# Kernel optimization log

Measured on AMD Instinct MI355X. Metric: run time of the kernel, lower is better.

## Reference

```python
import jax, jax.numpy as jnp
import numpy as np

NUM_HEADS = 8
EPS = 1e-5

def layer_norm(x, g, b):
    m = jnp.mean(x, axis=-1, keepdims=True)
    v = jnp.mean(jnp.square(x - m), axis=-1, keepdims=True)
    return (x - m) * jax.lax.rsqrt(v + EPS) * g + b

def setup_inputs() -> dict:
    key = jax.random.key(0)
    ks = jax.random.split(key, 16)
    B, C_enc, C_dec = 2, 512, 256
    H = W = D = 16
    d_ff = 4 * C_dec
    s = 0.02
    inp = {
        'encoder_feat': jax.random.normal(ks[0], (B, C_enc, H, W, D), jnp.float32),
        'decoder_feat': jax.random.normal(ks[1], (B, C_dec, H, W, D), jnp.float32),
        # projections stored as (in, out)
        'Wq': jax.random.normal(ks[2], (C_dec, C_dec), jnp.float32) * s,
        'bq': jnp.zeros((C_dec,), jnp.float32),
        'Wk': jax.random.normal(ks[3], (C_enc, C_dec), jnp.float32) * s,
        'bk': jnp.zeros((C_dec,), jnp.float32),
        'Wv': jax.random.normal(ks[4], (C_enc, C_dec), jnp.float32) * s,
        'bv': jnp.zeros((C_dec,), jnp.float32),
        'Wo': jax.random.normal(ks[5], (C_dec, C_dec), jnp.float32) * s,
        'bo': jnp.zeros((C_dec,), jnp.float32),
        'g_enc': jnp.ones((C_enc,), jnp.float32),
        'b_enc': jnp.zeros((C_enc,), jnp.float32),
        'g_dec': jnp.ones((C_dec,), jnp.float32),
        'b_dec': jnp.zeros((C_dec,), jnp.float32),
        'g_out': jnp.ones((C_dec,), jnp.float32),
        'b_out': jnp.zeros((C_dec,), jnp.float32),
        'W1': jax.random.normal(ks[6], (C_dec, d_ff), jnp.float32) * s,
        'b1': jnp.zeros((d_ff,), jnp.float32),
        'W2': jax.random.normal(ks[7], (d_ff, C_dec), jnp.float32) * s,
        'b2': jnp.zeros((C_dec,), jnp.float32),
    }
    return inp

def reference(encoder_feat, decoder_feat, Wq, bq, Wk, bk, Wv, bv, Wo, bo,
              g_enc, b_enc, g_dec, b_dec, g_out, b_out, W1, b1, W2, b2):
    B, C_dec, H, W, D = decoder_feat.shape
    h = NUM_HEADS
    hd = C_dec // h
    scale = hd ** -0.5
    # flatten spatial dims -> sequences [B, S, C]
    enc_seq = encoder_feat.reshape(B, encoder_feat.shape[1], -1).transpose(0, 2, 1)
    dec_seq = decoder_feat.reshape(B, C_dec, -1).transpose(0, 2, 1)
    enc_n = layer_norm(enc_seq, g_enc, b_enc)
    dec_n = layer_norm(dec_seq, g_dec, b_dec)
    Sq = dec_n.shape[1]
    Sk = enc_n.shape[1]
    Q = (dec_n @ Wq + bq).reshape(B, Sq, h, hd).transpose(0, 2, 1, 3)
    K = (enc_n @ Wk + bk).reshape(B, Sk, h, hd).transpose(0, 2, 1, 3)
    V = (enc_n @ Wv + bv).reshape(B, Sk, h, hd).transpose(0, 2, 1, 3)
    attn = jnp.einsum('bhqd,bhkd->bhqk', Q, K) * scale
    attn = jax.nn.softmax(attn, axis=-1)
    out = jnp.einsum('bhqk,bhkd->bhqd', attn, V)
    out = out.transpose(0, 2, 1, 3).reshape(B, Sq, C_dec)
    out = out @ Wo + bo
    out = dec_seq + out
    ffn = jax.nn.gelu(layer_norm(out, g_out, b_out) @ W1 + b1, approximate=False) @ W2 + b2
    out = out + ffn
    return out.transpose(0, 2, 1).reshape(B, C_dec, H, W, D)
```

## Files before the change

### kernel.cpp

```cpp
#include <hip/hip_runtime.h>
#include <hip/hip_bf16.h>
#include <math.h>
#include <stdint.h>

typedef __hip_bfloat16 bf16;
typedef __attribute__((ext_vector_type(8))) short short8;
typedef __attribute__((ext_vector_type(4))) short short4v;
typedef __attribute__((ext_vector_type(4))) float f32x4;
typedef __attribute__((ext_vector_type(4))) unsigned int uint32x4;
typedef __attribute__((ext_vector_type(2))) unsigned int uint32x2;

#define B_   2
#define S_   4096
#define CE   512
#define CD   256
#define DFF  1024
#define NH   8
#define HD   32

static __device__ __forceinline__ float b2f(bf16 x) { return __bfloat162float(x); }
static __device__ __forceinline__ bf16  f2b(float x) { return __float2bfloat16(x); }
static __device__ __forceinline__ short f2bs(float x) {
  bf16 h = f2b(x); return __builtin_bit_cast(short, h);
}
static __device__ __forceinline__ float s2f(short x) {
  return b2f(__builtin_bit_cast(bf16, x));
}
static __device__ __forceinline__ bool is_f32(const unsigned* graw) {
  return graw[0] == 0x3F800000u;
}

static __device__ __forceinline__ float exp2_(float x) {
#if __has_builtin(__builtin_amdgcn_exp2f)
  return __builtin_amdgcn_exp2f(x);
#else
  float r; asm("v_exp_f32 %0, %1" : "=v"(r) : "v"(x)); return r;
#endif
}
static __device__ __forceinline__ unsigned cvt_pk_bf16(float lo, float hi) {
  unsigned r;
  asm("v_cvt_pk_bf16_f32 %0, %1, %2" : "=v"(r) : "v"(lo), "v"(hi));
  return r;
}
static __device__ __forceinline__ void perm32(unsigned& a, unsigned& b) {
#if __has_builtin(__builtin_amdgcn_permlane32_swap)
  uint32x2 r = __builtin_amdgcn_permlane32_swap(a, b, false, false);
  a = r[0]; b = r[1];
#else
  asm("v_permlane32_swap_b32 %0, %1" : "+v"(a), "+v"(b));
#endif
}
static __device__ __forceinline__ void perm16(unsigned& a, unsigned& b) {
#if __has_builtin(__builtin_amdgcn_permlane16_swap)
  uint32x2 r = __builtin_amdgcn_permlane16_swap(a, b, false, false);
  a = r[0]; b = r[1];
#else
  asm("v_permlane16_swap_b32 %0, %1" : "+v"(a), "+v"(b));
#endif
}

#define GLD16(gptr, lptr) \
  __builtin_amdgcn_global_load_lds( \
      (const __attribute__((address_space(1))) unsigned int*)(gptr), \
      (__attribute__((address_space(3))) unsigned int*)(lptr), 16, 0, 0)

#define WAITVM(N) asm volatile("s_waitcnt vmcnt(" #N ")" ::: "memory")
#define BAR() __builtin_amdgcn_s_barrier()

struct PrepTab {
  const void* tsrc[6];
  bf16* tdst[6];
  int tK[6], tsStr[6], tdStr[6];
  float tscl[6];
  int tbase[7];
  const void* csrc[14];
  bf16* cdst[14];
  float cscl[14];
  int coff[15];
};

__global__ __launch_bounds__(256) void prep_kernel(
    PrepTab p, const unsigned* __restrict__ graw) {
  __shared__ bf16 tile[32][33];
  bool f32i = is_f32(graw);
  int blk = blockIdx.x;
  if (blk < p.tbase[6]) {
    int j = 0;
    #pragma unroll 1
    while (blk >= p.tbase[j + 1]) ++j;
    int local = blk - p.tbase[j];
    int ktiles = p.tK[j] >> 5;
    int nt = local / ktiles, kt = local - nt * ktiles;
    int k0 = kt * 32, n0 = nt * 32;
    const void* src = p.tsrc[j];
    bf16* dst = p.tdst[j];
    int sStr = p.tsStr[j], dStr = p.tdStr[j];
    float scl = p.tscl[j];
    int t = threadIdx.x;
    int tc = t & 31, tr = t >> 5;
    #pragma unroll
    for (int i = 0; i < 32; i += 8) {
      size_t idx = (size_t)(k0 + tr + i) * sStr + n0 + tc;
      float v = f32i ? ((const float*)src)[idx] : b2f(((const bf16*)src)[idx]);
      tile[tr + i][tc] = f2b(v * scl);
    }
    __syncthreads();
    #pragma unroll
    for (int i = 0; i < 32; i += 8)
      dst[(size_t)(n0 + tr + i) * dStr + k0 + tc] = tile[tc][tr + i];
  } else {
    int idx = (blk - p.tbase[6]) * 256 + threadIdx.x;
    int e4 = idx * 4;
    if (e4 >= p.coff[14]) return;
    int j = 0;
    #pragma unroll 1
    while (e4 >= p.coff[j + 1]) ++j;
    int local = e4 - p.coff[j];
    float v0, v1, v2, v3;
    if (f32i) {
      float4 f = *(const float4*)((const float*)p.csrc[j] + local);
      v0 = f.x; v1 = f.y; v2 = f.z; v3 = f.w;
    } else {
      short4v h = *(const short4v*)((const short*)p.csrc[j] + local);
      v0 = s2f(h[0]); v1 = s2f(h[1]); v2 = s2f(h[2]); v3 = s2f(h[3]);
    }
    float scl = p.cscl[j];
    short4v o;
    o[0] = f2bs(v0 * scl); o[1] = f2bs(v1 * scl);
    o[2] = f2bs(v2 * scl); o[3] = f2bs(v3 * scl);
    *(short4v*)((short*)p.cdst[j] + local) = o;
  }
}

struct LNCfg {
  const bf16 *x, *g, *bt;
  bf16 *xn, *xt;
  int C;
};

template<int CC, bool XT>
static __device__ __forceinline__ void ln_tile_body(
    const LNCfg& T, int b, int s0, short* sT, short* sG, short* sBt) {
  constexpr int P = CC + 8;
  constexpr int NJ = CC / 64;
  int t = threadIdx.x;
  if (t < CC / 8)      *(short8*)&sG[t * 8] = ((const short8*)T.g)[t];
  else if (t < CC / 4) *(short8*)&sBt[(t - CC/8) * 8] = ((const short8*)T.bt)[t - CC/8];

  int cg = t >> 2;
  int sq = (t & 3) * 8;
  const short* xg = (const short*)T.x + (size_t)b * CC * S_ + s0 + sq;
  short8 ld[NJ];
  #pragma unroll
  for (int ci = 0; ci < NJ; ++ci)
    ld[ci] = *(const short8*)(xg + (size_t)(ci * 64 + cg) * S_);
  #pragma unroll
  for (int ci = 0; ci < NJ; ++ci) {
    int c = ci * 64 + cg;
    #pragma unroll
    for (int j = 0; j < 8; ++j) {
      int s = sq + j;
      sT[s * P + (c ^ ((s & 24) << 1))] = ld[ci][j];
    }
  }
  __syncthreads();

  int w = t >> 6, l = t & 63;
  int grp = l >> 3, k = l & 7;
  int s = w * 8 + grp;
  int Z = (s & 24) << 1;
  short8 vals[NJ];
  float sum = 0.f, sq2 = 0.f;
  #pragma unroll
  for (int j = 0; j < NJ; ++j) {
    vals[j] = *(const short8*)&sT[s * P + j * 64 + ((k * 8) ^ Z)];
    #pragma unroll
    for (int i = 0; i < 8; ++i) {
      float v = s2f(vals[j][i]);
      sum += v; sq2 += v * v;
    }
  }
  #pragma unroll
  for (int off = 1; off < 8; off <<= 1) {
    sum += __shfl_xor(sum, off);
    sq2 += __shfl_xor(sq2, off);
  }
  float mean = sum * (1.f / CC);
  float rstd = rsqrtf(sq2 * (1.f / CC) - mean * mean + 1e-5f);
  size_t ro = ((size_t)b * S_ + s0 + s) * CC;
  #pragma unroll
  for (int j = 0; j < NJ; ++j) {
    int c0 = j * 64 + k * 8;
    short8 gv = *(const short8*)&sG[c0];
    short8 bv = *(const short8*)&sBt[c0];
    short8 o;
    #pragma unroll
    for (int i = 0; i < 8; ++i) {
      float v = s2f(vals[j][i]);
      o[i] = f2bs((v - mean) * rstd * s2f(gv[i]) + s2f(bv[i]));
    }
    *(short8*)((short*)T.xn + ro + c0) = o;
    if (XT) *(short8*)((short*)T.xt + ro + c0) = vals[j];
  }
}

__global__ __launch_bounds__(256) void ln_tile_kernel(LNCfg e, LNCfg d) {
  __shared__ __align__(16) short sT[32 * 520];
  __shared__ __align__(16) short sG[512], sBt[512];
  int gb = blockIdx.x;
  int local = gb & 255;
  int b = local >> 7, s0 = (local & 127) * 32;
  if (gb < 256) ln_tile_body<512, false>(e, b, s0, sT, sG, sBt);
  else          ln_tile_body<256, true>(d, b, s0, sT, sG, sBt);
}

__global__ __launch_bounds__(256) void ln_rows_kernel(
    const float* __restrict__ x, const bf16* __restrict__ g,
    const bf16* __restrict__ bt, bf16* __restrict__ xn, int C) {
  int wave = threadIdx.x >> 6, lane = threadIdx.x & 63;
  int row = blockIdx.x * 4 + wave;
  float4 v = *(const float4*)(x + (size_t)row * 256 + lane * 4);
  float sum = v.x + v.y + v.z + v.w;
  float sq = v.x * v.x + v.y * v.y + v.z * v.z + v.w * v.w;
  #pragma unroll
  for (int off = 1; off < 64; off <<= 1) {
    sum += __shfl_xor(sum, off);
    sq  += __shfl_xor(sq, off);
  }
  float mean = sum * (1.f / 256.f);
  float rstd = rsqrtf(sq * (1.f / 256.f) - mean * mean + 1e-5f);
  short4v gg = *(const short4v*)((const short*)g + lane * 4);
  short4v bb = *(const short4v*)((const short*)bt + lane * 4);
  short4v o;
  o[0] = f2bs((v.x - mean) * rstd * s2f(gg[0]) + s2f(bb[0]));
  o[1] = f2bs((v.y - mean) * rstd * s2f(gg[1]) + s2f(bb[1]));
  o[2] = f2bs((v.z - mean) * rstd * s2f(gg[2]) + s2f(bb[2]));
  o[3] = f2bs((v.w - mean) * rstd * s2f(gg[3]) + s2f(bb[3]));
  *(short4v*)((short*)xn + (size_t)row * 256 + lane * 4) = o;
}

__global__ __launch_bounds__(256) void gemm_mfma_kernel(
    const bf16* __restrict__ A, const bf16* __restrict__ Wt,
    const bf16* __restrict__ bias, int M, int N, int K,
    const bf16* __restrict__ resid_bf, const float* __restrict__ resid_f,
    bf16* __restrict__ out_bf, float* __restrict__ out_f,
    void* __restrict__ out_t, const unsigned* __restrict__ graw,
    int act, int resid_mode, int out_mode) {
  __shared__ __align__(16) short sA[3][128 * 32];
  __shared__ __align__(16) short sB[3][64 * 32];
  int m0 = blockIdx.y * 128, n0 = blockIdx.x * 64;
  int t = threadIdx.x;
  int w = t >> 6;
  int wm = w >> 1, wn = w & 1;
  int n16 = t & 15, quad = (t & 63) >> 4;
  int srow = t >> 2, skg = (t & 3) * 8;

  f32x4 acc[4][2] = {};
  const short* Ag = (const short*)A;
  const short* Wg = (const short*)Wt;
  const short* a0p = Ag + (size_t)(m0 + srow) * K + skg;
  const short* a1p = Ag + (size_t)(m0 + 64 + srow) * K + skg;
  const short* wp  = Wg + (size_t)(n0 + srow) * K + skg;

  auto stage = [&](int buf, int kk) {
    GLD16(a0p + kk, (char*)sA[buf] + t * 16);
    GLD16(a1p + kk, (char*)sA[buf] + t * 16 + 4096);
    GLD16(wp + kk,  (char*)sB[buf] + t * 16);
  };
  int nt = K >> 5;
  stage(0, 0);
  stage(1, 32);
  WAITVM(3);
  BAR();

  for (int ti = 0; ti < nt; ++ti) {
    int cur = ti % 3;
    bool pf = (ti + 2) < nt;
    if (pf) stage((ti + 2) % 3, (ti + 2) * 32);
    short8 af[4], bfr[2];
    #pragma unroll
    for (int ms = 0; ms < 4; ++ms)
      af[ms] = *(const short8*)&sA[cur][(wm * 64 + ms * 16 + n16) * 32 + quad * 8];
    #pragma unroll
    for (int ns = 0; ns < 2; ++ns)
      bfr[ns] = *(const short8*)&sB[cur][(wn * 32 + ns * 16 + n16) * 32 + quad * 8];
    #pragma unroll
    for (int ms = 0; ms < 4; ++ms)
      #pragma unroll
      for (int ns = 0; ns < 2; ++ns)
        acc[ms][ns] = __builtin_amdgcn_mfma_f32_16x16x32_bf16(
            af[ms], bfr[ns], acc[ms][ns], 0, 0, 0);
    if (pf) WAITVM(3); else WAITVM(0);
    BAR();
  }

  #pragma unroll
  for (int ms = 0; ms < 4; ++ms) {
    #pragma unroll
    for (int ns = 0; ns < 2; ++ns) {
      int col = n0 + wn * 32 + ns * 16 + n16;
      float bv = b2f(bias[col]);
      #pragma unroll
      for (int r = 0; r < 4; ++r) {
        int row = m0 + wm * 64 + ms * 16 + quad * 4 + r;
        float c = acc[ms][ns][r] + bv;
        if (act == 1) c = 0.5f * c * (1.f + erff(c * 0.70710678118654752f));
        size_t off = (size_t)row * N + col;
        if (resid_mode == 1)      c += b2f(resid_bf[off]);
        else if (resid_mode == 2) c += resid_f[off];
        if (out_f) out_f[off] = c;
        else       out_bf[off] = f2b(c);
      }
    }
  }
}

__global__ __launch_bounds__(256) void gemm64_mfma_kernel(
    const bf16* __restrict__ A, const bf16* __restrict__ Wt,
    const bf16* __restrict__ bias, int M, int N, int K,
    const bf16* __restrict__ resid_bf, const float* __restrict__ resid_f,
    bf16* __restrict__ out_bf, float* __restrict__ out_f,
    void* __restrict__ out_t, const unsigned* __restrict__ graw,
    int act, int resid_mode, int out_mode) {
  __shared__ __align__(16) short sA[3][64 * 32];
  __shared__ __align__(16) short sB[3][64 * 32];
  int m0 = blockIdx.y * 64, n0 = blockIdx.x * 64;
  int t = threadIdx.x;
  int w = t >> 6;
  int wm = w >> 1, wn = w & 1;
  int n16 = t & 15, quad = (t & 63) >> 4;
  int srow = t >> 2, skg = (t & 3) * 8;

  f32x4 acc[2][2] = {};
  const short* Ag = (const short*)A;
  const short* Wg = (const short*)Wt;
  const short* ap = Ag + (size_t)(m0 + srow) * K + skg;
  const short* wp = Wg + (size_t)(n0 + srow) * K + skg;

  auto stage = [&](int buf, int kk) {
    GLD16(ap + kk, (char*)sA[buf] + t * 16);
    GLD16(wp + kk, (char*)sB[buf] + t * 16);
  };
  int nt = K >> 5;
  stage(0, 0);
  stage(1, 32);
  WAITVM(2);
  BAR();

  for (int ti = 0; ti < nt; ++ti) {
    int cur = ti % 3;
    bool pf = (ti + 2) < nt;
    if (pf) stage((ti + 2) % 3, (ti + 2) * 32);
    short8 af[2], bfr[2];
    #pragma unroll
    for (int ms = 0; ms < 2; ++ms)
      af[ms] = *(const short8*)&sA[cur][(wm * 32 + ms * 16 + n16) * 32 + quad * 8];
    #pragma unroll
    for (int ns = 0; ns < 2; ++ns)
      bfr[ns] = *(const short8*)&sB[cur][(wn * 32 + ns * 16 + n16) * 32 + quad * 8];
    #pragma unroll
    for (int ms = 0; ms < 2; ++ms)
      #pragma unroll
      for (int ns = 0; ns < 2; ++ns)
        acc[ms][ns] = __builtin_amdgcn_mfma_f32_16x16x32_bf16(
            af[ms], bfr[ns], acc[ms][ns], 0, 0, 0);
    if (pf) WAITVM(2); else WAITVM(0);
    BAR();
  }

  if (out_mode == 3) {
    bool isf32 = is_f32(graw);
    #pragma unroll
    for (int ms = 0; ms < 2; ++ms) {
      int row0 = m0 + wm * 32 + ms * 16 + quad * 4;
      int bb = row0 >> 12, s = row0 & (S_ - 1);
      #pragma unroll
      for (int ns = 0; ns < 2; ++ns) {
        int col = n0 + wn * 32 + ns * 16 + n16;
        float bv = b2f(bias[col]);
        float cv[4];
        #pragma unroll
        for (int r = 0; r < 4; ++r)
          cv[r] = acc[ms][ns][r] + bv + resid_f[(size_t)(row0 + r) * N + col];
        size_t oidx = ((size_t)bb * CD + col) * S_ + s;
        if (isf32) {
          float4 v4 = {cv[0], cv[1], cv[2], cv[3]};
          *(float4*)((float*)out_t + oidx) = v4;
        } else {
          short4v v;
          #pragma unroll
          for (int r = 0; r < 4; ++r) v[r] = f2bs(cv[r]);
          *(short4v*)((bf16*)out_t + oidx) = v;
        }
      }
    }
    return;
  }

  #pragma unroll
  for (int ms = 0; ms < 2; ++ms) {
    #pragma unroll
    for (int ns = 0; ns < 2; ++ns) {
      int col = n0 + wn * 32 + ns * 16 + n16;
      float bv = b2f(bias[col]);
      #pragma unroll
      for (int r = 0; r < 4; ++r) {
        int row = m0 + wm * 32 + ms * 16 + quad * 4 + r;
        float c = acc[ms][ns][r] + bv;
        if (act == 1) c = 0.5f * c * (1.f + erff(c * 0.70710678118654752f));
        size_t off = (size_t)row * N + col;
        if (resid_mode == 1)      c += b2f(resid_bf[off]);
        else if (resid_mode == 2) c += resid_f[off];
        if (out_f) out_f[off] = c;
        else       out_bf[off] = f2b(c);
      }
    }
  }
}

__global__ __launch_bounds__(256) void qkv_kernel(
    const bf16* __restrict__ dec_n, const bf16* __restrict__ enc_n,
    const bf16* __restrict__ Wqt, const bf16* __restrict__ Wkvt,
    const bf16* __restrict__ bq, const bf16* __restrict__ bkv,
    bf16* __restrict__ Qm, bf16* __restrict__ Km, bf16* __restrict__ VT) {
  __shared__ __align__(16) short sA[3][64 * 32];
  __shared__ __align__(16) short sB[3][64 * 32];
  bool isQ = blockIdx.x < 4;
  const short* Ag = (const short*)(isQ ? dec_n : enc_n);
  const short* Wg = (const short*)(isQ ? Wqt : Wkvt);
  const bf16* bias = isQ ? bq : bkv;
  int K = isQ ? CD : CE;
  int n0 = isQ ? blockIdx.x * 64 : (blockIdx.x - 4) * 64;
  int m0 = blockIdx.y * 64;
  int t = threadIdx.x;
  int w = t >> 6;
  int wm = w >> 1, wn = w & 1;
  int n16 = t & 15, quad = (t & 63) >> 4;
  int srow = t >> 2, skg = (t & 3) * 8;

  f32x4 acc[2][2] = {};
  const short* ap = Ag + (size_t)(m0 + srow) * K + skg;
  const short* wp = Wg + (size_t)(n0 + srow) * K + skg;
  auto stage = [&](int buf, int kk) {
    GLD16(ap + kk, (char*)sA[buf] + t * 16);
    GLD16(wp + kk, (char*)sB[buf] + t * 16);
  };
  int nt = K >> 5;
  stage(0, 0);
  stage(1, 32);
  WAITVM(2);
  BAR();

  for (int ti = 0; ti < nt; ++ti) {
    int cur = ti % 3;
    bool pf = (ti + 2) < nt;
    if (pf) stage((ti + 2) % 3, (ti + 2) * 32);
    short8 af[2], bfr[2];
    #pragma unroll
    for (int ms = 0; ms < 2; ++ms)
      af[ms] = *(const short8*)&sA[cur][(wm * 32 + ms * 16 + n16) * 32 + quad * 8];
    #pragma unroll
    for (int ns = 0; ns < 2; ++ns)
      bfr[ns] = *(const short8*)&sB[cur][(wn * 32 + ns * 16 + n16) * 32 + quad * 8];
    #pragma unroll
    for (int ms = 0; ms < 2; ++ms)
      #pragma unroll
      for (int ns = 0; ns < 2; ++ns)
        acc[ms][ns] = __builtin_amdgcn_mfma_f32_16x16x32_bf16(
            af[ms], bfr[ns], acc[ms][ns], 0, 0, 0);
    if (pf) WAITVM(2); else WAITVM(0);
    BAR();
  }

  if (!isQ && n0 >= 256) {
    #pragma unroll
    for (int ms = 0; ms < 2; ++ms) {
      int row0 = m0 + wm * 32 + ms * 16 + quad * 4;
      int bb = row0 >> 12, s = row0 & (S_ - 1);
      #pragma unroll
      for (int ns = 0; ns < 2; ++ns) {
        int col = n0 + wn * 32 + ns * 16 + n16;
        float bv = b2f(bias[col]);
        short4v v;
        #pragma unroll
        for (int r = 0; r < 4; ++r) v[r] = f2bs(acc[ms][ns][r] + bv);
        *(short4v*)(VT + ((size_t)bb * CD + col - 256) * S_ + s) = v;
      }
    }
    return;
  }
  bf16* outp = isQ ? Qm : Km;
  #pragma unroll
  for (int ms = 0; ms < 2; ++ms) {
    #pragma unroll
    for (int ns = 0; ns < 2; ++ns) {
      int col = n0 + wn * 32 + ns * 16 + n16;
      float bv = b2f(bias[col]);
      #pragma unroll
      for (int r = 0; r < 4; ++r) {
        int row = m0 + wm * 32 + ms * 16 + quad * 4 + r;
        outp[(size_t)row * CD + col] = f2b(acc[ms][ns][r] + bv);
      }
    }
  }
}

__global__ __launch_bounds__(256) void attn_mfma_kernel(
    const bf16* __restrict__ Qm, const bf16* __restrict__ Km,
    const bf16* __restrict__ VT, float* __restrict__ Op0,
    float* __restrict__ Op1, float* __restrict__ Lp) {
  __shared__ __align__(16) short sKf[2][4][64][8];
  __shared__ __align__(16) short sVt[2][32][64];
  int b = blockIdx.z, h = blockIdx.y >> 1, half = blockIdx.y & 1;
  int q0 = blockIdx.x * 64;
  int t = threadIdx.x;
  int w = t >> 6, l = t & 63;
  int n = l & 15, quad = l >> 4;
  size_t bh = ((size_t)b * S_) * CD + h * HD;
  const short* kg = (const short*)Km + bh + (size_t)(w * 16 + n) * CD + quad * 8;
  const short* vtg = (const short*)VT +
      (size_t)(b * CD + h * HD + w * 8 + (l >> 3)) * S_ + ((l & 7) ^ ((l >> 3) & 7)) * 8;

  short8 qf = *(const short8*)((const short*)Qm + bh +
                               (size_t)(q0 + w * 16 + n) * CD + quad * 8);
  short8 ones8;
  #pragma unroll
  for (int i = 0; i < 8; ++i) ones8[i] = (short)0x3F80;

  f32x4 o0 = {0.f, 0.f, 0.f, 0.f}, o1 = {0.f, 0.f, 0.f, 0.f};
  f32x4 ol = {0.f, 0.f, 0.f, 0.f};

  auto stageKV = [&](int buf, int kk) {
    GLD16(kg + (size_t)kk * CD, &sKf[buf][w][l][0]);
    GLD16(vtg + kk, (short*)sVt[buf] + w * 512 + l * 8);
  };

  int kbeg = half * (S_ / 2), kend = kbeg + S_ / 2;
  stageKV(0, kbeg);
  WAITVM(0);
  BAR();
  int cur = 0;
  for (int k0 = kbeg; k0 < kend; k0 += 64) {
    if (k0 + 64 < kend) stageKV(cur ^ 1, k0 + 64);

    f32x4 sc[4];
    __builtin_amdgcn_s_setprio(1);
    #pragma unroll
    for (int st = 0; st < 4; ++st) {
      short8 kf = *(const short8*)&sKf[cur][st][l][0];
      f32x4 z = {0.f, 0.f, 0.f, 0.f};
      sc[st] = __builtin_amdgcn_mfma_f32_16x16x32_bf16(kf, qf, z, 0, 0, 0);
    }
    __builtin_amdgcn_s_setprio(0);

    unsigned Wd[4][2];
    #pragma unroll
    for (int st = 0; st < 4; ++st) {
      Wd[st][0] = cvt_pk_bf16(exp2_(sc[st][0]), exp2_(sc[st][1]));
      Wd[st][1] = cvt_pk_bf16(exp2_(sc[st][2]), exp2_(sc[st][3]));
    }
    uint32x4 pw0, pw1;
    #pragma unroll
    for (int m = 0; m < 2; ++m) {
      unsigned a0 = Wd[0][m], b0 = Wd[1][m];
      perm32(a0, b0); perm16(a0, b0);
      pw0[m] = a0; pw0[2 + m] = b0;
      unsigned a1 = Wd[2][m], b1 = Wd[3][m];
      perm32(a1, b1); perm16(a1, b1);
      pw1[m] = a1; pw1[2 + m] = b1;
    }
    short8 pf0 = __builtin_bit_cast(short8, pw0);
    short8 pf1 = __builtin_bit_cast(short8, pw1);

    int p80 = quad ^ (n & 7), p81 = (4 + quad) ^ (n & 7);
    short8 v00 = *(const short8*)&sVt[cur][n][p80 * 8];
    short8 v01 = *(const short8*)&sVt[cur][n][p81 * 8];
    short8 v10 = *(const short8*)&sVt[cur][16 + n][p80 * 8];
    short8 v11 = *(const short8*)&sVt[cur][16 + n][p81 * 8];

    __builtin_amdgcn_s_setprio(1);
    o0 = __builtin_amdgcn_mfma_f32_16x16x32_bf16(pf0, v00, o0, 0, 0, 0);
    o1 = __builtin_amdgcn_mfma_f32_16x16x32_bf16(pf0, v10, o1, 0, 0, 0);
    ol = __builtin_amdgcn_mfma_f32_16x16x32_bf16(pf0, ones8, ol, 0, 0, 0);
    o0 = __builtin_amdgcn_mfma_f32_16x16x32_bf16(pf1, v01, o0, 0, 0, 0);
    o1 = __builtin_amdgcn_mfma_f32_16x16x32_bf16(pf1, v11, o1, 0, 0, 0);
    ol = __builtin_amdgcn_mfma_f32_16x16x32_bf16(pf1, ones8, ol, 0, 0, 0);
    __builtin_amdgcn_s_setprio(0);

    WAITVM(0);
    BAR();
    cur ^= 1;
  }

  float* Opb = half ? Op1 : Op0;
  size_t pb = (size_t)b * S_;
  #pragma unroll
  for (int r = 0; r < 4; ++r) {
    int q = q0 + w * 16 + quad * 4 + r;
    float* orow = Opb + (pb + q) * CD + h * HD;
    orow[n]      = o0[r];
    orow[16 + n] = o1[r];
    if (n == 0) Lp[((size_t)(b * 2 + half) * S_ + q) * NH + h] = ol[r];
  }
}

__global__ __launch_bounds__(256) void attn_combine_kernel(
    const float* __restrict__ Op0, const float* __restrict__ Op1,
    const float* __restrict__ Lp, bf16* __restrict__ Am) {
  int idx = blockIdx.x * 256 + threadIdx.x;
  int c = (idx * 4) & (CD - 1);
  int bs = (idx * 4) >> 8;
  int s = bs & (S_ - 1), b = bs >> 12;
  int h = c >> 5;
  size_t row = (size_t)b * S_ + s;
  float l0 = Lp[((size_t)(b * 2 + 0) * S_ + s) * NH + h];
  float l1 = Lp[((size_t)(b * 2 + 1) * S_ + s) * NH + h];
  float inv = 1.f / (l0 + l1);
  float4 a = *(const float4*)&Op0[row * CD + c];
  float4 d = *(const float4*)&Op1[row * CD + c];
  short4v v;
  v[0] = f2bs((a.x + d.x) * inv);
  v[1] = f2bs((a.y + d.y) * inv);
  v[2] = f2bs((a.z + d.z) * inv);
  v[3] = f2bs((a.w + d.w) * inv);
  *(short4v*)&Am[row * CD + c] = v;
}

extern "C" void kernel_launch(void* const* d_in, const int* in_sizes, int n_in,
                              void* d_out, int out_size, void* d_ws, size_t ws_size,
                              hipStream_t stream) {
  const float kscale = 0.25503486f;
  const unsigned* graw = (const unsigned*)d_in[10];
  char* base = (char*)d_ws;
  size_t pos = 256;

  auto alloc = [&](size_t bytes) {
    char* p = base + pos; pos = (pos + bytes + 255) & ~(size_t)255; return p;
  };
  int cidx[14] = {0, 1, 3, 5, 7, 9, 10, 11, 12, 13, 14, 15, 17, 19};
  bf16* conv[20] = {};
  for (int k = 0; k < 14; ++k) {
    int i = cidx[k];
    conv[i] = (bf16*)alloc((size_t)2 * in_sizes[i]);
  }
  bf16* Wqt  = (bf16*)alloc((size_t)CD * CD * 2);
  bf16* Wkvt = (bf16*)alloc((size_t)CE * CE * 2);
  bf16* Wot  = (bf16*)alloc((size_t)CD * CD * 2);
  bf16* W1t  = (bf16*)alloc((size_t)DFF * CD * 2);
  bf16* W2t  = (bf16*)alloc((size_t)CD * DFF * 2);
  bf16* bkv  = (bf16*)alloc((size_t)CE * 2);
  conv[5] = bkv;
  conv[7] = bkv + CD;

  bf16*  enc_n = (bf16*) alloc((size_t)B_ * S_ * CE * 2);
  bf16*  dec_n = (bf16*) alloc((size_t)B_ * S_ * CD * 2);
  bf16*  Qm    = (bf16*) alloc((size_t)B_ * S_ * CD * 2);
  bf16*  Km    = (bf16*) alloc((size_t)B_ * S_ * CD * 2);
  bf16*  VT    = (bf16*) alloc((size_t)B_ * S_ * CD * 2);
  float* outm  = (float*)alloc((size_t)B_ * S_ * CD * 4);
  bf16*  hid   = (bf16*) alloc((size_t)B_ * S_ * DFF * 2);
  float* Lp    = (float*)alloc((size_t)B_ * 2 * S_ * NH * 4);
  bf16*  Am    = dec_n;
  bf16*  ln2   = Km;
  bf16*  dec_t = (bf16*)hid;
  float* Op0   = outm;
  float* Op1   = (float*)enc_n;

  PrepTab p;
  p.tsrc[0] = d_in[2];  p.tdst[0] = Wqt;            p.tK[0] = CD;  p.tsStr[0] = CD;  p.tdStr[0] = CD;  p.tscl[0] = kscale;
  p.tsrc[1] = d_in[4];  p.tdst[1] = Wkvt;           p.tK[1] = CE;  p.tsStr[1] = CD;  p.tdStr[1] = CE;  p.tscl[1] = 1.0f;
  p.tsrc[2] = d_in[6];  p.tdst[2] = Wkvt + CD * CE; p.tK[2] = CE;  p.tsStr[2] = CD;  p.tdStr[2] = CE;  p.tscl[2] = 1.0f;
  p.tsrc[3] = d_in[8];  p.tdst[3] = Wot;            p.tK[3] = CD;  p.tsStr[3] = CD;  p.tdStr[3] = CD;  p.tscl[3] = 1.0f;
  p.tsrc[4] = d_in[16]; p.tdst[4] = W1t;            p.tK[4] = CD;  p.tsStr[4] = DFF; p.tdStr[4] = CD;  p.tscl[4] = 1.0f;
  p.tsrc[5] = d_in[18]; p.tdst[5] = W2t;            p.tK[5] = DFF; p.tsStr[5] = CD;  p.tdStr[5] = DFF; p.tscl[5] = 1.0f;
  int tN[6] = {CD, CD, CD, CD, DFF, CD};
  p.tbase[0] = 0;
  for (int j = 0; j < 6; ++j)
    p.tbase[j + 1] = p.tbase[j] + (tN[j] / 32) * (p.tK[j] / 32);
  int coff = 0;
  for (int k = 0; k < 14; ++k) {
    int i = cidx[k];
    p.csrc[k] = d_in[i];
    p.cdst[k] = conv[i];
    p.cscl[k] = (i == 3) ? kscale : 1.0f;
    p.coff[k] = coff;
    coff += in_sizes[i];
  }
  p.coff[14] = coff;
  int prep_blocks = p.tbase[6] + (coff / 4 + 255) / 256;

  const bf16* enc_c = conv[0];
  const bf16* dec_c = conv[1];
  const bf16 *bq_c = conv[3], *bo_c = conv[9];
  const bf16 *ge_c = conv[10], *be_c = conv[11];
  const bf16 *gd_c = conv[12], *bd_c = conv[13];
  const bf16 *go_c = conv[14], *bo2_c = conv[15];
  const bf16 *b1_c = conv[17], *b2_c = conv[19];

  const int M = B_ * S_;

  prep_kernel<<<prep_blocks, 256, 0, stream>>>(p, graw);

  LNCfg lne = {enc_c, ge_c, be_c, enc_n, nullptr, CE};
  LNCfg lnd = {dec_c, gd_c, bd_c, dec_n, dec_t, CD};
  ln_tile_kernel<<<512, 256, 0, stream>>>(lne, lnd);

  qkv_kernel<<<dim3(12, M / 64), 256, 0, stream>>>(
      dec_n, enc_n, Wqt, Wkvt, bq_c, bkv, Qm, Km, VT);

  attn_mfma_kernel<<<dim3(S_ / 64, NH * 2, B_), 256, 0, stream>>>(Qm, Km, VT, Op0, Op1, Lp);
  attn_combine_kernel<<<(M * CD / 4) / 256, 256, 0, stream>>>(Op0, Op1, Lp, Am);

  gemm64_mfma_kernel<<<dim3(CD / 64, M / 64), 256, 0, stream>>>(
      Am, Wot, bo_c, M, CD, CD, dec_t, nullptr, nullptr, outm, nullptr, graw, 0, 1, 0);

  ln_rows_kernel<<<dim3(M / 4), 256, 0, stream>>>(outm, go_c, bo2_c, ln2, CD);

  gemm_mfma_kernel<<<dim3(DFF / 64, M / 128), 256, 0, stream>>>(
      ln2, W1t, b1_c, M, DFF, CD, nullptr, nullptr, hid, nullptr, nullptr, graw, 1, 0, 0);
  gemm64_mfma_kernel<<<dim3(CD / 64, M / 64), 256, 0, stream>>>(
      hid, W2t, b2_c, M, CD, DFF, nullptr, outm, nullptr, nullptr, d_out, graw, 0, 0, 3);
}
```

Baseline: 258.3 us.

## Process two query fragments per wave in attention to reuse staged K/V

Each attention block now covers 128 queries instead of 64, with every wave holding two 16-row Q fragments that share each K/V tile staged in shared memory. This halves the number of K/V global-to-LDS loads and barriers per query and gives the scheduler more independent MFMAs to interleave. In exchange each thread holds more accumulator registers, and the grid has half as many blocks (1024 instead of 2048), which could lower occupancy or leave load imbalance across CUs.

```diff
diff --git a/kernel.cpp b/kernel.cpp
--- a/kernel.cpp
+++ b/kernel.cpp
@@ -512,7 +512,7 @@
   __shared__ __align__(16) short sKf[2][4][64][8];
   __shared__ __align__(16) short sVt[2][32][64];
   int b = blockIdx.z, h = blockIdx.y >> 1, half = blockIdx.y & 1;
-  int q0 = blockIdx.x * 64;
+  int q0 = blockIdx.x * 128;
   int t = threadIdx.x;
   int w = t >> 6, l = t & 63;
   int n = l & 15, quad = l >> 4;
@@ -521,14 +521,22 @@
   const short* vtg = (const short*)VT +
       (size_t)(b * CD + h * HD + w * 8 + (l >> 3)) * S_ + ((l & 7) ^ ((l >> 3) & 7)) * 8;
 
-  short8 qf = *(const short8*)((const short*)Qm + bh +
-                               (size_t)(q0 + w * 16 + n) * CD + quad * 8);
+  short8 qf[2];
+  #pragma unroll
+  for (int f = 0; f < 2; ++f)
+    qf[f] = *(const short8*)((const short*)Qm + bh +
+                             (size_t)(q0 + w * 32 + f * 16 + n) * CD + quad * 8);
   short8 ones8;
   #pragma unroll
   for (int i = 0; i < 8; ++i) ones8[i] = (short)0x3F80;
 
-  f32x4 o0 = {0.f, 0.f, 0.f, 0.f}, o1 = {0.f, 0.f, 0.f, 0.f};
-  f32x4 ol = {0.f, 0.f, 0.f, 0.f};
+  f32x4 o0[2], o1[2], ol[2];
+  #pragma unroll
+  for (int f = 0; f < 2; ++f) {
+    o0[f] = f32x4{0.f, 0.f, 0.f, 0.f};
+    o1[f] = f32x4{0.f, 0.f, 0.f, 0.f};
+    ol[f] = f32x4{0.f, 0.f, 0.f, 0.f};
+  }
 
   auto stageKV = [&](int buf, int kk) {
     GLD16(kg + (size_t)kk * CD, &sKf[buf][w][l][0]);
@@ -543,34 +551,39 @@
   for (int k0 = kbeg; k0 < kend; k0 += 64) {
     if (k0 + 64 < kend) stageKV(cur ^ 1, k0 + 64);
 
-    f32x4 sc[4];
+    f32x4 sc[2][4];
     __builtin_amdgcn_s_setprio(1);
     #pragma unroll
     for (int st = 0; st < 4; ++st) {
       short8 kf = *(const short8*)&sKf[cur][st][l][0];
       f32x4 z = {0.f, 0.f, 0.f, 0.f};
-      sc[st] = __builtin_amdgcn_mfma_f32_16x16x32_bf16(kf, qf, z, 0, 0, 0);
+      sc[0][st] = __builtin_amdgcn_mfma_f32_16x16x32_bf16(kf, qf[0], z, 0, 0, 0);
+      sc[1][st] = __builtin_amdgcn_mfma_f32_16x16x32_bf16(kf, qf[1], z, 0, 0, 0);
     }
     __builtin_amdgcn_s_setprio(0);
 
-    unsigned Wd[4][2];
-    #pragma unroll
-    for (int st = 0; st < 4; ++st) {
-      Wd[st][0] = cvt_pk_bf16(exp2_(sc[st][0]), exp2_(sc[st][1]));
-      Wd[st][1] = cvt_pk_bf16(exp2_(sc[st][2]), exp2_(sc[st][3]));
-    }
-    uint32x4 pw0, pw1;
-    #pragma unroll
-    for (int m = 0; m < 2; ++m) {
-      unsigned a0 = Wd[0][m], b0 = Wd[1][m];
-      perm32(a0, b0); perm16(a0, b0);
-      pw0[m] = a0; pw0[2 + m] = b0;
-      unsigned a1 = Wd[2][m], b1 = Wd[3][m];
-      perm32(a1, b1); perm16(a1, b1);
-      pw1[m] = a1; pw1[2 + m] = b1;
-    }
-    short8 pf0 = __builtin_bit_cast(short8, pw0);
-    short8 pf1 = __builtin_bit_cast(short8, pw1);
+    short8 pf0[2], pf1[2];
+    #pragma unroll
+    for (int f = 0; f < 2; ++f) {
+      unsigned Wd[4][2];
+      #pragma unroll
+      for (int st = 0; st < 4; ++st) {
+        Wd[st][0] = cvt_pk_bf16(exp2_(sc[f][st][0]), exp2_(sc[f][st][1]));
+        Wd[st][1] = cvt_pk_bf16(exp2_(sc[f][st][2]), exp2_(sc[f][st][3]));
+      }
+      uint32x4 pw0, pw1;
+      #pragma unroll
+      for (int m = 0; m < 2; ++m) {
+        unsigned a0 = Wd[0][m], b0 = Wd[1][m];
+        perm32(a0, b0); perm16(a0, b0);
+        pw0[m] = a0; pw0[2 + m] = b0;
+        unsigned a1 = Wd[2][m], b1 = Wd[3][m];
+        perm32(a1, b1); perm16(a1, b1);
+        pw1[m] = a1; pw1[2 + m] = b1;
+      }
+      pf0[f] = __builtin_bit_cast(short8, pw0);
+      pf1[f] = __builtin_bit_cast(short8, pw1);
+    }
 
     int p80 = quad ^ (n & 7), p81 = (4 + quad) ^ (n & 7);
     short8 v00 = *(const short8*)&sVt[cur][n][p80 * 8];
@@ -579,12 +592,15 @@
     short8 v11 = *(const short8*)&sVt[cur][16 + n][p81 * 8];
 
     __builtin_amdgcn_s_setprio(1);
-    o0 = __builtin_amdgcn_mfma_f32_16x16x32_bf16(pf0, v00, o0, 0, 0, 0);
-    o1 = __builtin_amdgcn_mfma_f32_16x16x32_bf16(pf0, v10, o1, 0, 0, 0);
-    ol = __builtin_amdgcn_mfma_f32_16x16x32_bf16(pf0, ones8, ol, 0, 0, 0);
-    o0 = __builtin_amdgcn_mfma_f32_16x16x32_bf16(pf1, v01, o0, 0, 0, 0);
-    o1 = __builtin_amdgcn_mfma_f32_16x16x32_bf16(pf1, v11, o1, 0, 0, 0);
-    ol = __builtin_amdgcn_mfma_f32_16x16x32_bf16(pf1, ones8, ol, 0, 0, 0);
+    #pragma unroll
+    for (int f = 0; f < 2; ++f) {
+      o0[f] = __builtin_amdgcn_mfma_f32_16x16x32_bf16(pf0[f], v00, o0[f], 0, 0, 0);
+      o1[f] = __builtin_amdgcn_mfma_f32_16x16x32_bf16(pf0[f], v10, o1[f], 0, 0, 0);
+      ol[f] = __builtin_amdgcn_mfma_f32_16x16x32_bf16(pf0[f], ones8, ol[f], 0, 0, 0);
+      o0[f] = __builtin_amdgcn_mfma_f32_16x16x32_bf16(pf1[f], v01, o0[f], 0, 0, 0);
+      o1[f] = __builtin_amdgcn_mfma_f32_16x16x32_bf16(pf1[f], v11, o1[f], 0, 0, 0);
+      ol[f] = __builtin_amdgcn_mfma_f32_16x16x32_bf16(pf1[f], ones8, ol[f], 0, 0, 0);
+    }
     __builtin_amdgcn_s_setprio(0);
 
     WAITVM(0);
@@ -595,12 +611,15 @@
   float* Opb = half ? Op1 : Op0;
   size_t pb = (size_t)b * S_;
   #pragma unroll
-  for (int r = 0; r < 4; ++r) {
-    int q = q0 + w * 16 + quad * 4 + r;
-    float* orow = Opb + (pb + q) * CD + h * HD;
-    orow[n]      = o0[r];
-    orow[16 + n] = o1[r];
-    if (n == 0) Lp[((size_t)(b * 2 + half) * S_ + q) * NH + h] = ol[r];
+  for (int f = 0; f < 2; ++f) {
+    #pragma unroll
+    for (int r = 0; r < 4; ++r) {
+      int q = q0 + w * 32 + f * 16 + quad * 4 + r;
+      float* orow = Opb + (pb + q) * CD + h * HD;
+      orow[n]      = o0[f][r];
+      orow[16 + n] = o1[f][r];
+      if (n == 0) Lp[((size_t)(b * 2 + half) * S_ + q) * NH + h] = ol[f][r];
+    }
   }
 }
 
@@ -708,7 +727,7 @@
   qkv_kernel<<<dim3(12, M / 64), 256, 0, stream>>>(
       dec_n, enc_n, Wqt, Wkvt, bq_c, bkv, Qm, Km, VT);
 
-  attn_mfma_kernel<<<dim3(S_ / 64, NH * 2, B_), 256, 0, stream>>>(Qm, Km, VT, Op0, Op1, Lp);
+  attn_mfma_kernel<<<dim3(S_ / 128, NH * 2, B_), 256, 0, stream>>>(Qm, Km, VT, Op0, Op1, Lp);
   attn_combine_kernel<<<(M * CD / 4) / 256, 256, 0, stream>>>(Op0, Op1, Lp, Am);
 
   gemm64_mfma_kernel<<<dim3(CD / 64, M / 64), 256, 0, stream>>>(
```

After: 252.2 us. 1.02x faster.
